# Performance work log

Hardware: AMD Instinct MI355X
Metric: run time of the kernel (lower is better)

Reference implementation:

```python
import jax, jax.numpy as jnp
import numpy as np

BUCKET_SIZE = 256
LOOK_BACKWARD = 1
LOOK_FORWARD = 0  # causal


def look_around(x, backward, forward, pad_value):
    # x: (b, n_buckets, w, ...) -> (b, n_buckets, w*(backward+forward+1), ...)
    n = x.shape[1]
    pads = [(0, 0)] * x.ndim
    pads[1] = (backward, forward)
    p = jnp.pad(x, pads, constant_values=pad_value)
    return jnp.concatenate([p[:, i:i + n] for i in range(backward + forward + 1)], axis=2)


def setup_inputs() -> dict:
    key = jax.random.key(0)
    kq, kk, kv = jax.random.split(key, 3)
    shape = (2, 16, 4096, 64)  # [batch, heads, seq, head_dim]
    q = jax.random.normal(kq, shape, dtype=jnp.float32)
    k = jax.random.normal(kk, shape, dtype=jnp.float32)
    v = jax.random.normal(kv, shape, dtype=jnp.float32)
    return {"q": q, "k": k, "v": v}


def reference(q, k, v):
    shape = q.shape
    t, e = shape[-2], shape[-1]
    merge = lambda x: x.reshape(-1, t, e)
    q, k, v = merge(q), merge(k), merge(v)
    b = q.shape[0]
    buckets = t // BUCKET_SIZE

    bucket_fn = lambda x: x.reshape(b, buckets, BUCKET_SIZE, e)
    bq, bk, bv = bucket_fn(q), bucket_fn(k), bucket_fn(v)

    bk = look_around(bk, LOOK_BACKWARD, LOOK_FORWARD, 0.0)
    bv = look_around(bv, LOOK_BACKWARD, LOOK_FORWARD, 0.0)

    ticker = jnp.arange(t, dtype=jnp.int32).reshape(1, buckets, BUCKET_SIZE)
    bq_t = ticker  # (1, buckets, w)
    bq_k = look_around(ticker, LOOK_BACKWARD, LOOK_FORWARD, -1)  # (1, buckets, w*(lb+lf+1))

    dots = jnp.einsum('bnie,bnje->bnij', bq, bk) * (e ** -0.5)
    mask_value = -jnp.finfo(dots.dtype).max

    causal_mask = bq_t[:, :, :, None] < bq_k[:, :, None, :]
    pad_mask = (bq_k == -1)[:, :, None, :]
    dots = jnp.where(causal_mask | pad_mask, mask_value, dots)

    attn = jax.nn.softmax(dots, axis=-1)
    out = jnp.einsum('bnij,bnje->bnie', attn, bv)
    return out.reshape(shape)
```

## Files before the change

kernel.cpp:

```cpp
#include <hip/hip_runtime.h>

typedef __bf16 bf16x8 __attribute__((ext_vector_type(8)));
typedef float f32x16 __attribute__((ext_vector_type(16)));
typedef int i32x2 __attribute__((ext_vector_type(2)));
typedef unsigned int u32;

#define NCH 8

static __device__ __forceinline__ u32 cvt_pk_bf16(float lo, float hi) {
    u32 r;
    asm("v_cvt_pk_bf16_f32 %0, %1, %2" : "=v"(r) : "v"(lo), "v"(hi));
    return r;
}

__global__ __launch_bounds__(512, 4)
void local_attn_kernel(const float* __restrict__ qg, const float* __restrict__ kg,
                       const float* __restrict__ vg, float* __restrict__ og)
{
    __shared__ __align__(16) __bf16 sK[2][64][64];
    __shared__ __align__(16) u32 sVp[2][64][32];

    const int bid = ((blockIdx.x & 7) << 6) | (blockIdx.x >> 3);
    const int bh = bid >> 4, bi = bid & 15;
    const int tid = threadIdx.x, w = tid >> 6;
    const int lane = tid & 63, l31 = lane & 31, h = lane >> 5;

    const long long base = (long long)bh << 18;
    const float* qp = qg + base + ((long long)bi << 14);
    const float* kp = kg + base + (((long long)(bi - 1)) << 14);
    const float* vp = vg + base + (((long long)(bi - 1)) << 14);
    float*       op = og + base + ((long long)bi << 14);

    bf16x8 qf[4];
    {
        const float QS = 0.18033688011112042f;
        const float* qrow = qp + (w * 32 + l31) * 64 + 8 * h;
#pragma unroll
        for (int ks = 0; ks < 4; ++ks) {
            float4 f0 = *(const float4*)(qrow + ks * 16);
            float4 f1 = *(const float4*)(qrow + ks * 16 + 4);
            bf16x8 t;
            t[0] = (__bf16)(f0.x * QS); t[1] = (__bf16)(f0.y * QS);
            t[2] = (__bf16)(f0.z * QS); t[3] = (__bf16)(f0.w * QS);
            t[4] = (__bf16)(f1.x * QS); t[5] = (__bf16)(f1.y * QS);
            t[6] = (__bf16)(f1.z * QS); t[7] = (__bf16)(f1.w * QS);
            qf[ks] = t;
        }
    }

    f32x16 o0, o1;
#pragma unroll
    for (int i = 0; i < 16; ++i) { o0[i] = 0.f; o1[i] = 0.f; }
    float lsum = 0.f;

    const int skey = tid >> 3, stg = tid & 7;
    const int kslot = (stg ^ (skey & 7)) << 3;
    const int vkp = tid >> 4, vd0 = (tid & 15) * 4;
    const float* kA = kp + skey * 64 + stg * 8;
    const float* vA = vp + (2 * vkp) * 64 + vd0;

    const int c0 = (bi == 0) ? 4 : 0;
    const int qpos = w * 32 + l31;
    const int wlim = 32 * w + 287;

    int cur = 0;

    auto stage = [&](int c, int buf) {
        const float* ks_ = kA + c * (64 * 64);
        float4 k0 = *(const float4*)ks_;
        float4 k1 = *(const float4*)(ks_ + 4);
        const float* vs_ = vA + c * (64 * 64);
        float4 v0 = *(const float4*)vs_;
        float4 v1 = *(const float4*)(vs_ + 64);
        bf16x8 kv;
        kv[0] = (__bf16)k0.x; kv[1] = (__bf16)k0.y; kv[2] = (__bf16)k0.z; kv[3] = (__bf16)k0.w;
        kv[4] = (__bf16)k1.x; kv[5] = (__bf16)k1.y; kv[6] = (__bf16)k1.z; kv[7] = (__bf16)k1.w;
        *(bf16x8*)&sK[buf][skey][kslot] = kv;
        u32 p0 = cvt_pk_bf16(v0.x, v1.x);
        u32 p1 = cvt_pk_bf16(v0.y, v1.y);
        u32 p2 = cvt_pk_bf16(v0.z, v1.z);
        u32 p3 = cvt_pk_bf16(v0.w, v1.w);
        const int kq = vkp >> 2, kj = vkp & 3;
        sVp[buf][vd0 + 0][((kq ^ ((vd0 + 0) & 7)) << 2) + kj] = p0;
        sVp[buf][vd0 + 1][((kq ^ ((vd0 + 1) & 7)) << 2) + kj] = p1;
        sVp[buf][vd0 + 2][((kq ^ ((vd0 + 2) & 7)) << 2) + kj] = p2;
        sVp[buf][vd0 + 3][((kq ^ ((vd0 + 3) & 7)) << 2) + kj] = p3;
    };

    stage(c0, 0);

    for (int c = c0; c < NCH; ++c) {
        __syncthreads();
        if (c + 1 < NCH) stage(c + 1, cur ^ 1);

        const int kbase = c * 64;
#pragma unroll
        for (int kt = 0; kt < 2; ++kt) {
            if (kbase + 32 * kt > wlim) continue;

            const int key = kt * 32 + l31;
            const int ksw = key & 7;
            bf16x8 kfa[4];
#pragma unroll
            for (int ks = 0; ks < 4; ++ks)
                kfa[ks] = *(const bf16x8*)&sK[cur][key][((ks * 2 + h) ^ ksw) << 3];
            f32x16 s;
#pragma unroll
            for (int i = 0; i < 16; ++i) s[i] = 0.f;
#pragma unroll
            for (int ks = 0; ks < 4; ++ks)
                s = __builtin_amdgcn_mfma_f32_32x32x16_bf16(kfa[ks], qf[ks], s, 0, 0, 0);

            float pv[16];
            const int jb = kbase + 32 * kt + 4 * h;
            if (kbase + 32 * kt + 31 <= 32 * w + 256) {
#pragma unroll
                for (int r = 0; r < 16; ++r) {
                    pv[r] = __builtin_amdgcn_exp2f(s[r]);
                    lsum += pv[r];
                }
            } else {
#pragma unroll
                for (int r = 0; r < 16; ++r) {
                    const int j = jb + (r & 3) + 8 * (r >> 2);
                    float e = __builtin_amdgcn_exp2f(s[r]);
                    pv[r] = (j > qpos + 256) ? 0.f : e;
                    lsum += pv[r];
                }
            }

            u32 wds[8];
#pragma unroll
            for (int m = 0; m < 8; ++m)
                wds[m] = cvt_pk_bf16(pv[2 * m], pv[2 * m + 1]);

#pragma unroll
            for (int kis = 0; kis < 2; ++kis) {
                i32x2 r02 = __builtin_amdgcn_permlane32_swap(
                    (int)wds[4 * kis + 0], (int)wds[4 * kis + 2], false, false);
                i32x2 r13 = __builtin_amdgcn_permlane32_swap(
                    (int)wds[4 * kis + 1], (int)wds[4 * kis + 3], false, false);
                union { u32 u[4]; bf16x8 b; } pu;
                pu.u[0] = (u32)r02.x; pu.u[1] = (u32)r13.x;
                pu.u[2] = (u32)r02.y; pu.u[3] = (u32)r13.y;

                const int slot = ((kt * 2 + kis) * 2 + h) ^ (l31 & 7);
                bf16x8 vb0 = *(const bf16x8*)&sVp[cur][l31][slot << 2];
                bf16x8 vb1 = *(const bf16x8*)&sVp[cur][32 + l31][slot << 2];
                o0 = __builtin_amdgcn_mfma_f32_32x32x16_bf16(pu.b, vb0, o0, 0, 0, 0);
                o1 = __builtin_amdgcn_mfma_f32_32x32x16_bf16(pu.b, vb1, o1, 0, 0, 0);
            }
        }
        cur ^= 1;
    }

    lsum += __shfl_xor(lsum, 32, 64);
    const float inv = 1.0f / lsum;
#pragma unroll
    for (int r = 0; r < 16; ++r) {
        const int qr = (r & 3) + 8 * (r >> 2) + 4 * h;
        const float iq = __shfl(inv, qr, 64);
        float* orow = op + (w * 32 + qr) * 64;
        orow[l31]      = o0[r] * iq;
        orow[32 + l31] = o1[r] * iq;
    }
}

extern "C" void kernel_launch(void* const* d_in, const int* in_sizes, int n_in,
                              void* d_out, int out_size, void* d_ws, size_t ws_size,
                              hipStream_t stream) {
    const float* q = (const float*)d_in[0];
    const float* k = (const float*)d_in[1];
    const float* v = (const float*)d_in[2];
    float* out = (float*)d_out;
    local_attn_kernel<<<dim3(512), dim3(512), 0, stream>>>(q, k, v, out);
}
```

Baseline: 35.91 us.

## Stage 128-key chunks with register prefetch deferred past compute and new V swizzle

Doubles the key/value chunk to 128 keys, which halves the number of loop iterations and barriers. Global loads for the next chunk are issued before the MFMA work, and the LDS writes are deferred until after it, so memory latency overlaps with compute. The V LDS layout gets an extra XOR swizzle term to avoid bank conflicts with the wider rows, and K conversion now uses packed cvt instructions. The cost is double the LDS footprint and more live registers, which could reduce occupancy under launch_bounds(512,4).

New measurement: 58.55 us. 1.63x slower.

```diff
diff --git a/kernel.cpp b/kernel.cpp
--- a/kernel.cpp
+++ b/kernel.cpp
@@ -5,7 +5,7 @@
 typedef int i32x2 __attribute__((ext_vector_type(2)));
 typedef unsigned int u32;
 
-#define NCH 8
+#define NCH 4
 
 static __device__ __forceinline__ u32 cvt_pk_bf16(float lo, float hi) {
     u32 r;
@@ -17,8 +17,8 @@
 void local_attn_kernel(const float* __restrict__ qg, const float* __restrict__ kg,
                        const float* __restrict__ vg, float* __restrict__ og)
 {
-    __shared__ __align__(16) __bf16 sK[2][64][64];
-    __shared__ __align__(16) u32 sVp[2][64][32];
+    __shared__ __align__(16) __bf16 sK[2][128][64];
+    __shared__ __align__(16) u32 sVp[2][64][64];
 
     const int bid = ((blockIdx.x & 7) << 6) | (blockIdx.x >> 3);
     const int bh = bid >> 4, bi = bid & 15;
@@ -56,47 +56,57 @@
     const int skey = tid >> 3, stg = tid & 7;
     const int kslot = (stg ^ (skey & 7)) << 3;
     const int vkp = tid >> 4, vd0 = (tid & 15) * 4;
-    const float* kA = kp + skey * 64 + stg * 8;
-    const float* vA = vp + (2 * vkp) * 64 + vd0;
 
-    const int c0 = (bi == 0) ? 4 : 0;
+    const int c0 = (bi == 0) ? 2 : 0;
     const int qpos = w * 32 + l31;
-    const int wlim = 32 * w + 287;
 
     int cur = 0;
+    union F4 { float4 v; float f[4]; };
+    F4 kr[2][2], vr[2][2];
 
-    auto stage = [&](int c, int buf) {
-        const float* ks_ = kA + c * (64 * 64);
-        float4 k0 = *(const float4*)ks_;
-        float4 k1 = *(const float4*)(ks_ + 4);
-        const float* vs_ = vA + c * (64 * 64);
-        float4 v0 = *(const float4*)vs_;
-        float4 v1 = *(const float4*)(vs_ + 64);
-        bf16x8 kv;
-        kv[0] = (__bf16)k0.x; kv[1] = (__bf16)k0.y; kv[2] = (__bf16)k0.z; kv[3] = (__bf16)k0.w;
-        kv[4] = (__bf16)k1.x; kv[5] = (__bf16)k1.y; kv[6] = (__bf16)k1.z; kv[7] = (__bf16)k1.w;
-        *(bf16x8*)&sK[buf][skey][kslot] = kv;
-        u32 p0 = cvt_pk_bf16(v0.x, v1.x);
-        u32 p1 = cvt_pk_bf16(v0.y, v1.y);
-        u32 p2 = cvt_pk_bf16(v0.z, v1.z);
-        u32 p3 = cvt_pk_bf16(v0.w, v1.w);
-        const int kq = vkp >> 2, kj = vkp & 3;
-        sVp[buf][vd0 + 0][((kq ^ ((vd0 + 0) & 7)) << 2) + kj] = p0;
-        sVp[buf][vd0 + 1][((kq ^ ((vd0 + 1) & 7)) << 2) + kj] = p1;
-        sVp[buf][vd0 + 2][((kq ^ ((vd0 + 2) & 7)) << 2) + kj] = p2;
-        sVp[buf][vd0 + 3][((kq ^ ((vd0 + 3) & 7)) << 2) + kj] = p3;
+    auto stage_load = [&](int c) {
+#pragma unroll
+        for (int a = 0; a < 2; ++a) {
+            const float* ks_ = kp + (c * 128 + skey + 64 * a) * 64 + stg * 8;
+            kr[a][0].v = *(const float4*)ks_;
+            kr[a][1].v = *(const float4*)(ks_ + 4);
+            const float* vs_ = vp + (c * 128 + 2 * (vkp + 32 * a)) * 64 + vd0;
+            vr[a][0].v = *(const float4*)vs_;
+            vr[a][1].v = *(const float4*)(vs_ + 64);
+        }
+    };
+    auto stage_write = [&](int buf) {
+#pragma unroll
+        for (int a = 0; a < 2; ++a) {
+            union { u32 u[4]; bf16x8 b; } kv;
+            kv.u[0] = cvt_pk_bf16(kr[a][0].f[0], kr[a][0].f[1]);
+            kv.u[1] = cvt_pk_bf16(kr[a][0].f[2], kr[a][0].f[3]);
+            kv.u[2] = cvt_pk_bf16(kr[a][1].f[0], kr[a][1].f[1]);
+            kv.u[3] = cvt_pk_bf16(kr[a][1].f[2], kr[a][1].f[3]);
+            *(bf16x8*)&sK[buf][skey + 64 * a][kslot] = kv.b;
+            const int kp2 = vkp + 32 * a, G = kp2 >> 2, j = kp2 & 3;
+#pragma unroll
+            for (int i = 0; i < 4; ++i) {
+                const int row = vd0 + i;
+                const int sl = G ^ (row & 7) ^ ((row >> 2) & 7);
+                sVp[buf][row][(sl << 2) + j] = cvt_pk_bf16(vr[a][0].f[i], vr[a][1].f[i]);
+            }
+        }
     };
 
-    stage(c0, 0);
+    stage_load(c0);
+    stage_write(0);
 
     for (int c = c0; c < NCH; ++c) {
         __syncthreads();
-        if (c + 1 < NCH) stage(c + 1, cur ^ 1);
+        const bool pf = (c + 1 < NCH);
+        if (pf) stage_load(c + 1);
 
-        const int kbase = c * 64;
+        const int kbase_c = c * 128;
 #pragma unroll
-        for (int kt = 0; kt < 2; ++kt) {
-            if (kbase + 32 * kt > wlim) continue;
+        for (int kt = 0; kt < 4; ++kt) {
+            const int kb0 = kbase_c + kt * 32;
+            if (kb0 > 32 * w + 287) continue;
 
             const int key = kt * 32 + l31;
             const int ksw = key & 7;
@@ -112,8 +122,8 @@
                 s = __builtin_amdgcn_mfma_f32_32x32x16_bf16(kfa[ks], qf[ks], s, 0, 0, 0);
 
             float pv[16];
-            const int jb = kbase + 32 * kt + 4 * h;
-            if (kbase + 32 * kt + 31 <= 32 * w + 256) {
+            const int jb = kb0 + 4 * h;
+            if (kb0 + 31 <= 32 * w + 256) {
 #pragma unroll
                 for (int r = 0; r < 16; ++r) {
                     pv[r] = __builtin_amdgcn_exp2f(s[r]);
@@ -144,13 +154,16 @@
                 pu.u[0] = (u32)r02.x; pu.u[1] = (u32)r13.x;
                 pu.u[2] = (u32)r02.y; pu.u[3] = (u32)r13.y;
 
-                const int slot = ((kt * 2 + kis) * 2 + h) ^ (l31 & 7);
-                bf16x8 vb0 = *(const bf16x8*)&sVp[cur][l31][slot << 2];
-                bf16x8 vb1 = *(const bf16x8*)&sVp[cur][32 + l31][slot << 2];
+                const int G = (kt * 2 + kis) * 2 + h;
+                const int sl = G ^ (l31 & 7) ^ ((l31 >> 2) & 7);
+                bf16x8 vb0 = *(const bf16x8*)&sVp[cur][l31][sl << 2];
+                bf16x8 vb1 = *(const bf16x8*)&sVp[cur][32 + l31][sl << 2];
                 o0 = __builtin_amdgcn_mfma_f32_32x32x16_bf16(pu.b, vb0, o0, 0, 0, 0);
                 o1 = __builtin_amdgcn_mfma_f32_32x32x16_bf16(pu.b, vb1, o1, 0, 0, 0);
             }
         }
+
+        if (pf) stage_write(cur ^ 1);
         cur ^= 1;
     }
 
```

## Split staging into early global loads and late LDS writes, re-swizzle V tile

Applied to the files above, without the earlier changes.

The next chunk's K/V global loads are now issued before the compute of the current chunk, and the bf16 conversion and LDS stores are deferred until after the MFMA work. This hides global memory latency behind compute. It also changes the V tile's XOR swizzle to include row bits, to reduce LDS bank conflicts, and packs K with cvt_pk_bf16. In exchange it holds 16 extra registers live across the compute loop, which could hurt occupancy at the 512x4 launch bound.

Result: faster. 34.15 us (-4.9%).

```diff
diff --git a/kernel.cpp b/kernel.cpp
--- a/kernel.cpp
+++ b/kernel.cpp
@@ -56,6 +56,7 @@
     const int skey = tid >> 3, stg = tid & 7;
     const int kslot = (stg ^ (skey & 7)) << 3;
     const int vkp = tid >> 4, vd0 = (tid & 15) * 4;
+    const int vkq = vkp >> 2, vj = vkp & 3;
     const float* kA = kp + skey * 64 + stg * 8;
     const float* vA = vp + (2 * vkp) * 64 + vd0;
 
@@ -64,39 +65,49 @@
     const int wlim = 32 * w + 287;
 
     int cur = 0;
+    float4 k0r, k1r, v0r, v1r;
 
-    auto stage = [&](int c, int buf) {
-        const float* ks_ = kA + c * (64 * 64);
-        float4 k0 = *(const float4*)ks_;
-        float4 k1 = *(const float4*)(ks_ + 4);
-        const float* vs_ = vA + c * (64 * 64);
-        float4 v0 = *(const float4*)vs_;
-        float4 v1 = *(const float4*)(vs_ + 64);
-        bf16x8 kv;
-        kv[0] = (__bf16)k0.x; kv[1] = (__bf16)k0.y; kv[2] = (__bf16)k0.z; kv[3] = (__bf16)k0.w;
-        kv[4] = (__bf16)k1.x; kv[5] = (__bf16)k1.y; kv[6] = (__bf16)k1.z; kv[7] = (__bf16)k1.w;
-        *(bf16x8*)&sK[buf][skey][kslot] = kv;
-        u32 p0 = cvt_pk_bf16(v0.x, v1.x);
-        u32 p1 = cvt_pk_bf16(v0.y, v1.y);
-        u32 p2 = cvt_pk_bf16(v0.z, v1.z);
-        u32 p3 = cvt_pk_bf16(v0.w, v1.w);
-        const int kq = vkp >> 2, kj = vkp & 3;
-        sVp[buf][vd0 + 0][((kq ^ ((vd0 + 0) & 7)) << 2) + kj] = p0;
-        sVp[buf][vd0 + 1][((kq ^ ((vd0 + 1) & 7)) << 2) + kj] = p1;
-        sVp[buf][vd0 + 2][((kq ^ ((vd0 + 2) & 7)) << 2) + kj] = p2;
-        sVp[buf][vd0 + 3][((kq ^ ((vd0 + 3) & 7)) << 2) + kj] = p3;
-    };
+#define STAGE_LOAD(c) do {                                   \
+        const float* ks_ = kA + (c) * (64 * 64);             \
+        k0r = *(const float4*)ks_;                           \
+        k1r = *(const float4*)(ks_ + 4);                     \
+        const float* vs_ = vA + (c) * (64 * 64);             \
+        v0r = *(const float4*)vs_;                           \
+        v1r = *(const float4*)(vs_ + 64);                    \
+    } while (0)
 
-    stage(c0, 0);
+#define STAGE_WRITE(buf) do {                                                     \
+        union { u32 u[4]; bf16x8 b; } kv_;                                        \
+        kv_.u[0] = cvt_pk_bf16(k0r.x, k0r.y);                                     \
+        kv_.u[1] = cvt_pk_bf16(k0r.z, k0r.w);                                     \
+        kv_.u[2] = cvt_pk_bf16(k1r.x, k1r.y);                                     \
+        kv_.u[3] = cvt_pk_bf16(k1r.z, k1r.w);                                     \
+        *(bf16x8*)&sK[buf][skey][kslot] = kv_.b;                                  \
+        {                                                                         \
+            const int r0 = vd0,     s0 = vkq ^ (r0 & 7) ^ ((r0 >> 2) & 7);        \
+            const int r1 = vd0 + 1, s1 = vkq ^ (r1 & 7) ^ ((r1 >> 2) & 7);        \
+            const int r2 = vd0 + 2, s2 = vkq ^ (r2 & 7) ^ ((r2 >> 2) & 7);        \
+            const int r3 = vd0 + 3, s3 = vkq ^ (r3 & 7) ^ ((r3 >> 2) & 7);        \
+            sVp[buf][r0][(s0 << 2) + vj] = cvt_pk_bf16(v0r.x, v1r.x);             \
+            sVp[buf][r1][(s1 << 2) + vj] = cvt_pk_bf16(v0r.y, v1r.y);             \
+            sVp[buf][r2][(s2 << 2) + vj] = cvt_pk_bf16(v0r.z, v1r.z);             \
+            sVp[buf][r3][(s3 << 2) + vj] = cvt_pk_bf16(v0r.w, v1r.w);             \
+        }                                                                         \
+    } while (0)
+
+    STAGE_LOAD(c0);
+    STAGE_WRITE(0);
 
     for (int c = c0; c < NCH; ++c) {
         __syncthreads();
-        if (c + 1 < NCH) stage(c + 1, cur ^ 1);
+        const bool pf = (c + 1 < NCH);
+        if (pf) STAGE_LOAD(c + 1);
 
         const int kbase = c * 64;
 #pragma unroll
         for (int kt = 0; kt < 2; ++kt) {
-            if (kbase + 32 * kt > wlim) continue;
+            const int kb0 = kbase + 32 * kt;
+            if (kb0 > wlim) continue;
 
             const int key = kt * 32 + l31;
             const int ksw = key & 7;
@@ -112,8 +123,8 @@
                 s = __builtin_amdgcn_mfma_f32_32x32x16_bf16(kfa[ks], qf[ks], s, 0, 0, 0);
 
             float pv[16];
-            const int jb = kbase + 32 * kt + 4 * h;
-            if (kbase + 32 * kt + 31 <= 32 * w + 256) {
+            const int jb = kb0 + 4 * h;
+            if (kb0 + 31 <= 32 * w + 256) {
 #pragma unroll
                 for (int r = 0; r < 16; ++r) {
                     pv[r] = __builtin_amdgcn_exp2f(s[r]);
@@ -144,13 +155,16 @@
                 pu.u[0] = (u32)r02.x; pu.u[1] = (u32)r13.x;
                 pu.u[2] = (u32)r02.y; pu.u[3] = (u32)r13.y;
 
-                const int slot = ((kt * 2 + kis) * 2 + h) ^ (l31 & 7);
-                bf16x8 vb0 = *(const bf16x8*)&sVp[cur][l31][slot << 2];
-                bf16x8 vb1 = *(const bf16x8*)&sVp[cur][32 + l31][slot << 2];
+                const int G = (kt * 2 + kis) * 2 + h;
+                const int sl = G ^ (l31 & 7) ^ ((l31 >> 2) & 7);
+                bf16x8 vb0 = *(const bf16x8*)&sVp[cur][l31][sl << 2];
+                bf16x8 vb1 = *(const bf16x8*)&sVp[cur][32 + l31][sl << 2];
                 o0 = __builtin_amdgcn_mfma_f32_32x32x16_bf16(pu.b, vb0, o0, 0, 0, 0);
                 o1 = __builtin_amdgcn_mfma_f32_32x32x16_bf16(pu.b, vb1, o1, 0, 0, 0);
             }
         }
+
+        if (pf) STAGE_WRITE(cur ^ 1);
         cur ^= 1;
     }
 
```
